# Optimization experiments

Measured on AMD Instinct MI355X. Metric: run time of the kernel, lower is better.

Reference implementation:

```python
import jax, jax.numpy as jnp
from jax import lax
import numpy as np

VOCAB = 50000
EMBED = 300
UNITS = 512          # num_nodes[0]
D1 = 1024            # num_nodes[1]
D2 = 1024            # num_nodes[2]
NUM_CLASSES = 20
B, T = 64, 512


def setup_inputs() -> dict:
    key = jax.random.key(0)
    ks = jax.random.split(key, 12)
    s = 0.02
    return {
        "tokens": jax.random.randint(ks[0], (B, T), 0, VOCAB),
        "emb": jax.random.normal(ks[1], (VOCAB, EMBED), jnp.float32) * s,
        "Wx": jax.random.normal(ks[2], (EMBED, 4 * UNITS), jnp.float32) * s,
        "Wh": jax.random.normal(ks[3], (UNITS, 4 * UNITS), jnp.float32) * s,
        "b": jnp.zeros((4 * UNITS,), jnp.float32),
        "W1": jax.random.normal(ks[4], (UNITS, D1), jnp.float32) * s,
        "b1": jnp.zeros((D1,), jnp.float32),
        "W2": jax.random.normal(ks[5], (D1, D2), jnp.float32) * s,
        "b2": jnp.zeros((D2,), jnp.float32),
        "Wo": jax.random.normal(ks[6], (D2, NUM_CLASSES), jnp.float32) * s,
        "bo": jnp.zeros((NUM_CLASSES,), jnp.float32),
    }


def reference(tokens, emb, Wx, Wh, b, W1, b1, W2, b2, Wo, bo):
    # Embedding with mask_zero=True: token 0 timesteps are masked -> LSTM skips
    # the state update (Keras semantics).
    mask = (tokens != 0)                               # [B, T]
    x = emb[tokens]                                    # [B, T, E]
    units = Wh.shape[0]
    # Precompute input contribution to the gates (parallel over time).
    xg = jnp.einsum('bte,eg->btg', x, Wx) + b          # [B, T, 4U]

    def step(carry, inp):
        h, c = carry
        g_x, m = inp                                   # [B,4U], [B]
        g = g_x + h @ Wh                               # [B, 4U]
        i, f, cc, o = jnp.split(g, 4, axis=-1)         # Keras gate order i,f,c,o
        i = jax.nn.sigmoid(i)
        f = jax.nn.sigmoid(f)
        o = jax.nn.sigmoid(o)
        # activation='relu' replaces tanh in candidate and output transform.
        c_new = f * c + i * jax.nn.relu(cc)
        h_new = o * jax.nn.relu(c_new)
        m = m[:, None]
        h = jnp.where(m, h_new, h)
        c = jnp.where(m, c_new, c)
        return (h, c), None

    h0 = jnp.zeros((tokens.shape[0], units), x.dtype)
    (h, _), _ = lax.scan(step, (h0, h0),
                         (jnp.swapaxes(xg, 0, 1), mask.T))  # scan over T

    h = jax.nn.relu(h @ W1 + b1)
    h = jax.nn.relu(h @ W2 + b2)
    return jax.nn.softmax(h @ Wo + bo)
```

## Files before the change

### kernel.cpp

```cpp
#include <hip/hip_runtime.h>
#include <hip/hip_bf16.h>

#define B_   64
#define T_   512
#define E_   300
#define U_   512
#define G4_  2048
#define D1_  1024
#define D2_  1024
#define NC_  20
#define KP_  320

typedef __bf16 bf16x8 __attribute__((ext_vector_type(8)));
typedef float  f32x4  __attribute__((ext_vector_type(4)));

__device__ __forceinline__ float sigmoidf_(float x) { return 1.0f / (1.0f + __expf(-x)); }

__device__ __forceinline__ void gl_lds16(const void* g, void* l) {
    __builtin_amdgcn_global_load_lds(
        (const __attribute__((address_space(1))) unsigned int*)g,
        (__attribute__((address_space(3))) unsigned int*)l, 16, 0, 0);
}

__global__ void init_kernel(unsigned int* __restrict__ hz, int* __restrict__ flags) {
    int idx = blockIdx.x * 256 + threadIdx.x;
    if (idx < (B_ * U_ / 2)) hz[idx] = 0u;
    if (idx < 256) flags[idx] = 0;
}

__global__ __launch_bounds__(256) void prep_wxT(const float* __restrict__ Wx,
                                                __hip_bfloat16* __restrict__ wxT) {
    __shared__ __hip_bfloat16 t[64][65];
    const int n0 = blockIdx.x * 64;
    const int k0 = blockIdx.y * 64;
    const int tid = threadIdx.x;
    for (int i = tid; i < 4096; i += 256) {
        int r = i >> 6, c = i & 63;
        int k = k0 + r;
        float v = (k < E_) ? Wx[(size_t)k * G4_ + n0 + c] : 0.f;
        t[r][c] = __float2bfloat16(v);
    }
    __syncthreads();
    for (int i = tid; i < 4096; i += 256) {
        int r = i >> 6, c = i & 63;
        wxT[(size_t)(n0 + r) * KP_ + k0 + c] = t[c][r];
    }
}

__global__ __launch_bounds__(256) void prep_xb(const int* __restrict__ tokens,
                                               const float* __restrict__ emb,
                                               __hip_bfloat16* __restrict__ xb) {
    const int row = blockIdx.x * 4 + (threadIdx.x >> 6);
    const int ln  = threadIdx.x & 63;
    const int tok = tokens[row];
    const float* src = emb + (size_t)tok * E_;
    __hip_bfloat16* dst = xb + (size_t)row * KP_;
    for (int k = ln; k < KP_; k += 64)
        dst[k] = (k < E_) ? __float2bfloat16(src[k]) : __float2bfloat16(0.f);
}

__global__ __launch_bounds__(256) void xg_gemm(const __hip_bfloat16* __restrict__ xb,
                                               const __hip_bfloat16* __restrict__ wxT,
                                               const float* __restrict__ bias,
                                               __hip_bfloat16* __restrict__ xg) {
    const int n0g = blockIdx.x * 128;
    const int bt0 = blockIdx.y * 128;
    const int tid = threadIdx.x;
    const int w   = tid >> 6;
    const int ln  = tid & 63;
    const int fn  = ln & 15;
    const int quad = ln >> 4;
    const int m0  = (w >> 1) * 64;
    const int n0w = (w & 1) * 64;

    __shared__ __align__(16) __hip_bfloat16 As[128 * 32];
    __shared__ __align__(16) __hip_bfloat16 Bs[128 * 32];

    f32x4 acc[4][4];
    #pragma unroll
    for (int im = 0; im < 4; ++im)
        #pragma unroll
        for (int in = 0; in < 4; ++in)
            acc[im][in] = (f32x4){0.f, 0.f, 0.f, 0.f};

    const __hip_bfloat16* ga = xb  + (size_t)(bt0 + w * 32 + (ln >> 2)) * KP_ + (ln & 3) * 8;
    const __hip_bfloat16* gb = wxT + (size_t)(n0g + w * 32 + (ln >> 2)) * KP_ + (ln & 3) * 8;

    for (int kt = 0; kt < KP_ / 32; ++kt) {
        gl_lds16(ga,             &As[(w * 32) * 32]);
        gl_lds16(ga + 16 * KP_,  &As[(w * 32 + 16) * 32]);
        gl_lds16(gb,             &Bs[(w * 32) * 32]);
        gl_lds16(gb + 16 * KP_,  &Bs[(w * 32 + 16) * 32]);
        ga += 32; gb += 32;
        __syncthreads();

        bf16x8 af[4], bf[4];
        #pragma unroll
        for (int im = 0; im < 4; ++im)
            af[im] = *(const bf16x8*)&As[(m0 + im * 16 + fn) * 32 + quad * 8];
        #pragma unroll
        for (int in = 0; in < 4; ++in)
            bf[in] = *(const bf16x8*)&Bs[(n0w + in * 16 + fn) * 32 + quad * 8];
        #pragma unroll
        for (int im = 0; im < 4; ++im)
            #pragma unroll
            for (int in = 0; in < 4; ++in)
                acc[im][in] = __builtin_amdgcn_mfma_f32_16x16x32_bf16(
                    af[im], bf[in], acc[im][in], 0, 0, 0);
        __syncthreads();
    }

    #pragma unroll
    for (int in = 0; in < 4; ++in) {
        const int n = n0g + n0w + in * 16 + fn;
        const float bv = bias[n];
        #pragma unroll
        for (int im = 0; im < 4; ++im) {
            #pragma unroll
            for (int r = 0; r < 4; ++r) {
                int m = bt0 + m0 + im * 16 + quad * 4 + r;
                int bb = m >> 9, tt = m & 511;
                xg[(size_t)(tt * B_ + bb) * G4_ + n] =
                    __float2bfloat16(acc[im][in][r] + bv);
            }
        }
    }
}

__global__ __launch_bounds__(256) void lstm_kernel(const __hip_bfloat16* __restrict__ xg,
                                                   const int* __restrict__ tokens,
                                                   const float* __restrict__ Wh,
                                                   __hip_bfloat16* __restrict__ hbuf,
                                                   int* __restrict__ flags) {
    const int tid  = threadIdx.x;
    const int lane = tid & 63;
    const int wave = tid >> 6;
    const int x  = blockIdx.x & 7;
    const int r_ = blockIdx.x >> 3;
    const int ub = x * 8 + (r_ & 7);
    const int g  = r_ >> 3;
    const int u0 = ub * 8;

    __shared__ __align__(16) __hip_bfloat16 whsT[32][520];
    __shared__ __align__(16) __hip_bfloat16 hs[16][520];
    __shared__ float gbuf[16][32];
    __shared__ unsigned mask_lds[16][16];

    for (int idx = tid; idx < 32 * 512; idx += 256) {
        int c = idx & 31, k = idx >> 5;
        int col = ((c >> 3) << 9) + u0 + (c & 7);
        whsT[c][k] = __float2bfloat16(Wh[(size_t)k * G4_ + col]);
    }
    {
        int m = tid >> 4, wi = tid & 15;
        const int4* tp = (const int4*)(tokens + (size_t)(g * 16 + m) * T_ + wi * 32);
        unsigned bits = 0;
        #pragma unroll
        for (int q = 0; q < 8; ++q) {
            int4 v = tp[q];
            bits |= (v.x != 0 ? 1u : 0u) << (q * 4 + 0);
            bits |= (v.y != 0 ? 1u : 0u) << (q * 4 + 1);
            bits |= (v.z != 0 ? 1u : 0u) << (q * 4 + 2);
            bits |= (v.w != 0 ? 1u : 0u) << (q * 4 + 3);
        }
        mask_lds[m][wi] = bits;
    }

    float c0 = 0.f, c1 = 0.f, h0 = 0.f, h1 = 0.f;
    int* gflags = flags + g * 64;

    const int fn   = lane & 15;
    const int quad = lane >> 4;
    const int fc   = wave * 16 + fn;
    const int fcol = ((fc >> 3) << 9) + u0 + (fc & 7);

    __syncthreads();

    for (int s = 0; s < T_; ++s) {
        float xv[4];
        if (wave < 2) {
            #pragma unroll
            for (int r = 0; r < 4; ++r)
                xv[r] = __bfloat162float(
                    xg[(size_t)(s * B_ + g * 16 + quad * 4 + r) * G4_ + fcol]);
        }

        if (s > 0) {
            if (tid < 64) {
                while (__hip_atomic_load(&gflags[tid], __ATOMIC_RELAXED,
                                         __HIP_MEMORY_SCOPE_AGENT) < s)
                    __builtin_amdgcn_s_sleep(2);
            }
            __syncthreads();
        }

        {
            const uint4* hp = (const uint4*)(hbuf + (size_t)((s & 1) * B_ + g * 16) * U_);
            uint4 t0, t1, t2, t3;
            asm volatile(
                "global_load_dwordx4 %0, %4, off sc0 sc1\n\t"
                "global_load_dwordx4 %1, %5, off sc0 sc1\n\t"
                "global_load_dwordx4 %2, %6, off sc0 sc1\n\t"
                "s_waitcnt vmcnt(0)\n\t"
                "global_load_dwordx4 %3, %7, off sc0 sc1\n\t"
                "s_waitcnt vmcnt(0)"
                : "=&v"(t0), "=&v"(t1), "=&v"(t2), "=&v"(t3)
                : "v"(hp + tid), "v"(hp + tid + 256), "v"(hp + tid + 512),
                  "v"(hp + tid + 768)
                : "memory");
            int i0 = tid;        *((uint4*)&hs[i0 >> 6][(i0 & 63) * 8]) = t0;
            int i1 = tid + 256;  *((uint4*)&hs[i1 >> 6][(i1 & 63) * 8]) = t1;
            int i2 = tid + 512;  *((uint4*)&hs[i2 >> 6][(i2 & 63) * 8]) = t2;
            int i3 = tid + 768;  *((uint4*)&hs[i3 >> 6][(i3 & 63) * 8]) = t3;
        }
        __syncthreads();

        if (wave < 2) {
            f32x4 acc;
            #pragma unroll
            for (int r = 0; r < 4; ++r) acc[r] = xv[r];
            const __hip_bfloat16* arow = &hs[fn][quad * 8];
            const __hip_bfloat16* brow = &whsT[fc][quad * 8];
            #pragma unroll
            for (int kk = 0; kk < 16; ++kk) {
                bf16x8 av = *(const bf16x8*)(arow + kk * 32);
                bf16x8 bv = *(const bf16x8*)(brow + kk * 32);
                acc = __builtin_amdgcn_mfma_f32_16x16x32_bf16(av, bv, acc, 0, 0, 0);
            }
            #pragma unroll
            for (int r = 0; r < 4; ++r)
                gbuf[quad * 4 + r][fc] = acc[r];
        }
        __syncthreads();

        if (tid < 64) {
            const int m  = tid >> 2;
            const int u2 = (tid & 3) << 1;
            float gi0 = sigmoidf_(gbuf[m][u2]),      gi1 = sigmoidf_(gbuf[m][u2 + 1]);
            float gf0 = sigmoidf_(gbuf[m][8 + u2]),  gf1 = sigmoidf_(gbuf[m][9 + u2]);
            float gc0 = gbuf[m][16 + u2],            gc1 = gbuf[m][17 + u2];
            float go0 = sigmoidf_(gbuf[m][24 + u2]), go1 = sigmoidf_(gbuf[m][25 + u2]);
            float cn0 = gf0 * c0 + gi0 * fmaxf(gc0, 0.f);
            float cn1 = gf1 * c1 + gi1 * fmaxf(gc1, 0.f);
            float hn0 = go0 * fmaxf(cn0, 0.f);
            float hn1 = go1 * fmaxf(cn1, 0.f);
            if ((mask_lds[m][s >> 5] >> (s & 31)) & 1u) {
                c0 = cn0; c1 = cn1; h0 = hn0; h1 = hn1;
            }
            __hip_bfloat162 hv;
            hv.x = __float2bfloat16(h0);
            hv.y = __float2bfloat16(h1);
            unsigned wv;
            __builtin_memcpy(&wv, &hv, 4);
            unsigned* dst = (unsigned*)hbuf +
                (((((s + 1) & 1) * B_ + g * 16 + m) * U_ + u0 + u2) >> 1);
            __hip_atomic_store(dst, wv, __ATOMIC_RELAXED, __HIP_MEMORY_SCOPE_AGENT);
        }
        __syncthreads();
        if (tid == 0)
            __hip_atomic_store(&gflags[ub], s + 1, __ATOMIC_RELAXED,
                               __HIP_MEMORY_SCOPE_AGENT);
    }
}

__global__ __launch_bounds__(256) void fc1_kernel(const __hip_bfloat16* __restrict__ h,
                                                  const float* __restrict__ W,
                                                  const float* __restrict__ bias,
                                                  float* __restrict__ y) {
    int b = blockIdx.x >> 2, ch = blockIdx.x & 3;
    __shared__ float xrow[U_];
    for (int i = threadIdx.x; i < U_; i += 256)
        xrow[i] = __bfloat162float(h[b * U_ + i]);
    __syncthreads();
    int n = ch * 256 + threadIdx.x;
    float acc = 0.f;
    #pragma unroll 4
    for (int k = 0; k < U_; ++k) acc = fmaf(xrow[k], W[(size_t)k * D1_ + n], acc);
    y[b * D1_ + n] = fmaxf(acc + bias[n], 0.f);
}

__global__ __launch_bounds__(256) void fc2_kernel(const float* __restrict__ x,
                                                  const float* __restrict__ W,
                                                  const float* __restrict__ bias,
                                                  float* __restrict__ y) {
    int b = blockIdx.x >> 2, ch = blockIdx.x & 3;
    __shared__ float xrow[D1_];
    for (int i = threadIdx.x; i < D1_; i += 256) xrow[i] = x[b * D1_ + i];
    __syncthreads();
    int n = ch * 256 + threadIdx.x;
    float acc = 0.f;
    #pragma unroll 4
    for (int k = 0; k < D1_; ++k) acc = fmaf(xrow[k], W[(size_t)k * D2_ + n], acc);
    y[b * D2_ + n] = fmaxf(acc + bias[n], 0.f);
}

__global__ __launch_bounds__(64) void out_kernel(const float* __restrict__ h2,
                                                 const float* __restrict__ Wo,
                                                 const float* __restrict__ bo,
                                                 float* __restrict__ out) {
    int b = blockIdx.x;
    __shared__ float xrow[D2_];
    __shared__ float lg[NC_];
    __shared__ float red[2];
    for (int i = threadIdx.x; i < D2_; i += 64) xrow[i] = h2[b * D2_ + i];
    __syncthreads();
    if (threadIdx.x < NC_) {
        float a = bo[threadIdx.x];
        for (int k = 0; k < D2_; ++k) a = fmaf(xrow[k], Wo[k * NC_ + threadIdx.x], a);
        lg[threadIdx.x] = a;
    }
    __syncthreads();
    if (threadIdx.x == 0) {
        float mx = lg[0];
        for (int c = 1; c < NC_; ++c) mx = fmaxf(mx, lg[c]);
        float sm = 0.f;
        for (int c = 0; c < NC_; ++c) sm += expf(lg[c] - mx);
        red[0] = mx; red[1] = 1.0f / sm;
    }
    __syncthreads();
    if (threadIdx.x < NC_)
        out[b * NC_ + threadIdx.x] = expf(lg[threadIdx.x] - red[0]) * red[1];
}

extern "C" void kernel_launch(void* const* d_in, const int* in_sizes, int n_in,
                              void* d_out, int out_size, void* d_ws, size_t ws_size,
                              hipStream_t stream) {
    const int*   tokens = (const int*)d_in[0];
    const float* emb    = (const float*)d_in[1];
    const float* Wx     = (const float*)d_in[2];
    const float* Wh     = (const float*)d_in[3];
    const float* b      = (const float*)d_in[4];
    const float* W1     = (const float*)d_in[5];
    const float* b1     = (const float*)d_in[6];
    const float* W2     = (const float*)d_in[7];
    const float* b2     = (const float*)d_in[8];
    const float* Wo     = (const float*)d_in[9];
    const float* bo     = (const float*)d_in[10];
    float* out = (float*)d_out;

    char* ws = (char*)d_ws;
    const size_t XG_BYTES   = (size_t)T_ * B_ * G4_ * 2;
    const size_t HBUF_BYTES = (size_t)2 * B_ * U_ * 2;
    __hip_bfloat16* xg   = (__hip_bfloat16*)ws;
    __hip_bfloat16* hbuf = (__hip_bfloat16*)(ws + XG_BYTES);
    int* flags           = (int*)(ws + XG_BYTES + HBUF_BYTES);
    char* p = ws + XG_BYTES + HBUF_BYTES + 1024;
    float* h1            = (float*)p;                 p += (size_t)B_ * D1_ * 4;
    float* h2            = (float*)p;                 p += (size_t)B_ * D2_ * 4;
    __hip_bfloat16* xb   = (__hip_bfloat16*)p;        p += (size_t)B_ * T_ * KP_ * 2;
    __hip_bfloat16* wxT  = (__hip_bfloat16*)p;

    init_kernel<<<64, 256, 0, stream>>>((unsigned int*)hbuf, flags);
    prep_wxT<<<dim3(32, 5), 256, 0, stream>>>(Wx, wxT);
    prep_xb<<<(B_ * T_) / 4, 256, 0, stream>>>(tokens, emb, xb);
    xg_gemm<<<dim3(16, 256), 256, 0, stream>>>(xb, wxT, b, xg);
    lstm_kernel<<<256, 256, 0, stream>>>(xg, tokens, Wh, hbuf, flags);
    fc1_kernel<<<256, 256, 0, stream>>>(hbuf, W1, b1, h1);
    fc2_kernel<<<256, 256, 0, stream>>>(h1, W2, b2, h2);
    out_kernel<<<64, 64, 0, stream>>>(h2, Wo, bo, out);
}
```

Before: 1.655 ms.

## Replace per-block flag barrier with step-tagged hidden-state words in LSTM

Each hidden-state word now carries the timestep it belongs to, written as a 64-bit atomic store. Consumer blocks spin directly on the h data until every tag matches the step. This removes the separate flag polling, the extra block barrier and the flag store on every timestep, cutting round-trip latency in the cross-block recurrence. In exchange the exchange buffer doubles in size, every poll moves more bytes, and correctness depends on the 64-bit stores being observed atomically.

```diff
diff --git a/kernel.cpp b/kernel.cpp
--- a/kernel.cpp
+++ b/kernel.cpp
@@ -22,10 +22,10 @@
         (__attribute__((address_space(3))) unsigned int*)l, 16, 0, 0);
 }
 
-__global__ void init_kernel(unsigned int* __restrict__ hz, int* __restrict__ flags) {
+__global__ void init_kernel(uint4* __restrict__ hch) {
     int idx = blockIdx.x * 256 + threadIdx.x;
-    if (idx < (B_ * U_ / 2)) hz[idx] = 0u;
-    if (idx < 256) flags[idx] = 0;
+    int g = idx >> 11, j = idx & 2047;
+    hch[(size_t)g * 4096 + j] = (uint4){0u, 0u, 0u, 0u};
 }
 
 __global__ __launch_bounds__(256) void prep_wxT(const float* __restrict__ Wx,
@@ -94,19 +94,19 @@
         ga += 32; gb += 32;
         __syncthreads();
 
-        bf16x8 af[4], bf[4];
+        bf16x8 af[4], bfr[4];
         #pragma unroll
         for (int im = 0; im < 4; ++im)
             af[im] = *(const bf16x8*)&As[(m0 + im * 16 + fn) * 32 + quad * 8];
         #pragma unroll
         for (int in = 0; in < 4; ++in)
-            bf[in] = *(const bf16x8*)&Bs[(n0w + in * 16 + fn) * 32 + quad * 8];
+            bfr[in] = *(const bf16x8*)&Bs[(n0w + in * 16 + fn) * 32 + quad * 8];
         #pragma unroll
         for (int im = 0; im < 4; ++im)
             #pragma unroll
             for (int in = 0; in < 4; ++in)
                 acc[im][in] = __builtin_amdgcn_mfma_f32_16x16x32_bf16(
-                    af[im], bf[in], acc[im][in], 0, 0, 0);
+                    af[im], bfr[in], acc[im][in], 0, 0, 0);
         __syncthreads();
     }
 
@@ -130,8 +130,8 @@
 __global__ __launch_bounds__(256) void lstm_kernel(const __hip_bfloat16* __restrict__ xg,
                                                    const int* __restrict__ tokens,
                                                    const float* __restrict__ Wh,
-                                                   __hip_bfloat16* __restrict__ hbuf,
-                                                   int* __restrict__ flags) {
+                                                   uint4* __restrict__ hch,
+                                                   __hip_bfloat16* __restrict__ hfin) {
     const int tid  = threadIdx.x;
     const int lane = tid & 63;
     const int wave = tid >> 6;
@@ -166,8 +166,15 @@
         mask_lds[m][wi] = bits;
     }
 
-    float c0 = 0.f, c1 = 0.f, h0 = 0.f, h1 = 0.f;
-    int* gflags = flags + g * 64;
+    float cst[4] = {0.f, 0.f, 0.f, 0.f};
+    float hst[4] = {0.f, 0.f, 0.f, 0.f};
+    const int um = tid >> 1;
+    const int uu = (tid & 1) * 4;
+
+    const int sm  = tid >> 4;
+    const int sjb = tid & 15;
+
+    uint4* gbase = hch + (size_t)g * 4096;
 
     const int fn   = lane & 15;
     const int quad = lane >> 4;
@@ -185,33 +192,40 @@
                     xg[(size_t)(s * B_ + g * 16 + quad * 4 + r) * G4_ + fcol]);
         }
 
-        if (s > 0) {
-            if (tid < 64) {
-                while (__hip_atomic_load(&gflags[tid], __ATOMIC_RELAXED,
-                                         __HIP_MEMORY_SCOPE_AGENT) < s)
-                    __builtin_amdgcn_s_sleep(2);
+        {
+            const uint4* cp = gbase + (s & 1) * 2048 + sm * 128 + sjb;
+            uint4 v0, v1, v2, v3, v4, v5, v6, v7;
+            const unsigned exp = (unsigned)s;
+            for (;;) {
+                asm volatile(
+                    "global_load_dwordx4 %0, %8, off sc0 sc1\n\t"
+                    "global_load_dwordx4 %1, %8, off offset:256 sc0 sc1\n\t"
+                    "global_load_dwordx4 %2, %8, off offset:512 sc0 sc1\n\t"
+                    "global_load_dwordx4 %3, %8, off offset:768 sc0 sc1\n\t"
+                    "global_load_dwordx4 %4, %8, off offset:1024 sc0 sc1\n\t"
+                    "global_load_dwordx4 %5, %8, off offset:1280 sc0 sc1\n\t"
+                    "global_load_dwordx4 %6, %8, off offset:1536 sc0 sc1\n\t"
+                    "global_load_dwordx4 %7, %8, off offset:1792 sc0 sc1\n\t"
+                    "s_waitcnt vmcnt(0)"
+                    : "=&v"(v0), "=&v"(v1), "=&v"(v2), "=&v"(v3),
+                      "=&v"(v4), "=&v"(v5), "=&v"(v6), "=&v"(v7)
+                    : "v"(cp)
+                    : "memory");
+                bool ok = (v0.y == exp) & (v0.w == exp) & (v1.y == exp) & (v1.w == exp)
+                        & (v2.y == exp) & (v2.w == exp) & (v3.y == exp) & (v3.w == exp)
+                        & (v4.y == exp) & (v4.w == exp) & (v5.y == exp) & (v5.w == exp)
+                        & (v6.y == exp) & (v6.w == exp) & (v7.y == exp) & (v7.w == exp);
+                if (ok) break;
+                __builtin_amdgcn_s_sleep(1);
             }
-            __syncthreads();
-        }
-
-        {
-            const uint4* hp = (const uint4*)(hbuf + (size_t)((s & 1) * B_ + g * 16) * U_);
-            uint4 t0, t1, t2, t3;
-            asm volatile(
-                "global_load_dwordx4 %0, %4, off sc0 sc1\n\t"
-                "global_load_dwordx4 %1, %5, off sc0 sc1\n\t"
-                "global_load_dwordx4 %2, %6, off sc0 sc1\n\t"
-                "s_waitcnt vmcnt(0)\n\t"
-                "global_load_dwordx4 %3, %7, off sc0 sc1\n\t"
-                "s_waitcnt vmcnt(0)"
-                : "=&v"(t0), "=&v"(t1), "=&v"(t2), "=&v"(t3)
-                : "v"(hp + tid), "v"(hp + tid + 256), "v"(hp + tid + 512),
-                  "v"(hp + tid + 768)
-                : "memory");
-            int i0 = tid;        *((uint4*)&hs[i0 >> 6][(i0 & 63) * 8]) = t0;
-            int i1 = tid + 256;  *((uint4*)&hs[i1 >> 6][(i1 & 63) * 8]) = t1;
-            int i2 = tid + 512;  *((uint4*)&hs[i2 >> 6][(i2 & 63) * 8]) = t2;
-            int i3 = tid + 768;  *((uint4*)&hs[i3 >> 6][(i3 & 63) * 8]) = t3;
+            *(uint2*)&hs[sm][(sjb +   0) * 4] = (uint2){v0.x, v0.z};
+            *(uint2*)&hs[sm][(sjb +  16) * 4] = (uint2){v1.x, v1.z};
+            *(uint2*)&hs[sm][(sjb +  32) * 4] = (uint2){v2.x, v2.z};
+            *(uint2*)&hs[sm][(sjb +  48) * 4] = (uint2){v3.x, v3.z};
+            *(uint2*)&hs[sm][(sjb +  64) * 4] = (uint2){v4.x, v4.z};
+            *(uint2*)&hs[sm][(sjb +  80) * 4] = (uint2){v5.x, v5.z};
+            *(uint2*)&hs[sm][(sjb +  96) * 4] = (uint2){v6.x, v6.z};
+            *(uint2*)&hs[sm][(sjb + 112) * 4] = (uint2){v7.x, v7.z};
         }
         __syncthreads();
 
@@ -233,33 +247,34 @@
         }
         __syncthreads();
 
-        if (tid < 64) {
-            const int m  = tid >> 2;
-            const int u2 = (tid & 3) << 1;
-            float gi0 = sigmoidf_(gbuf[m][u2]),      gi1 = sigmoidf_(gbuf[m][u2 + 1]);
-            float gf0 = sigmoidf_(gbuf[m][8 + u2]),  gf1 = sigmoidf_(gbuf[m][9 + u2]);
-            float gc0 = gbuf[m][16 + u2],            gc1 = gbuf[m][17 + u2];
-            float go0 = sigmoidf_(gbuf[m][24 + u2]), go1 = sigmoidf_(gbuf[m][25 + u2]);
-            float cn0 = gf0 * c0 + gi0 * fmaxf(gc0, 0.f);
-            float cn1 = gf1 * c1 + gi1 * fmaxf(gc1, 0.f);
-            float hn0 = go0 * fmaxf(cn0, 0.f);
-            float hn1 = go1 * fmaxf(cn1, 0.f);
-            if ((mask_lds[m][s >> 5] >> (s & 31)) & 1u) {
-                c0 = cn0; c1 = cn1; h0 = hn0; h1 = hn1;
+        if (tid < 32) {
+            const unsigned m = mask_lds[um][s >> 5] >> (s & 31) & 1u;
+            #pragma unroll
+            for (int q = 0; q < 4; ++q) {
+                float gi = sigmoidf_(gbuf[um][uu + q]);
+                float gf = sigmoidf_(gbuf[um][8 + uu + q]);
+                float gc = gbuf[um][16 + uu + q];
+                float go = sigmoidf_(gbuf[um][24 + uu + q]);
+                float cn = gf * cst[q] + gi * fmaxf(gc, 0.f);
+                float hn = go * fmaxf(cn, 0.f);
+                if (m) { cst[q] = cn; hst[q] = hn; }
             }
-            __hip_bfloat162 hv;
-            hv.x = __float2bfloat16(h0);
-            hv.y = __float2bfloat16(h1);
-            unsigned wv;
-            __builtin_memcpy(&wv, &hv, 4);
-            unsigned* dst = (unsigned*)hbuf +
-                (((((s + 1) & 1) * B_ + g * 16 + m) * U_ + u0 + u2) >> 1);
-            __hip_atomic_store(dst, wv, __ATOMIC_RELAXED, __HIP_MEMORY_SCOPE_AGENT);
-        }
-        __syncthreads();
-        if (tid == 0)
-            __hip_atomic_store(&gflags[ub], s + 1, __ATOMIC_RELAXED,
-                               __HIP_MEMORY_SCOPE_AGENT);
+            __hip_bfloat162 p0, p1;
+            p0.x = __float2bfloat16(hst[0]); p0.y = __float2bfloat16(hst[1]);
+            p1.x = __float2bfloat16(hst[2]); p1.y = __float2bfloat16(hst[3]);
+            unsigned d0, d1;
+            __builtin_memcpy(&d0, &p0, 4);
+            __builtin_memcpy(&d1, &p1, 4);
+            const unsigned long long tagw = (unsigned long long)(unsigned)(s + 1) << 32;
+            unsigned long long h01 = tagw | d0;
+            unsigned long long h23 = tagw | d1;
+            unsigned long long* dst = (unsigned long long*)
+                (gbase + ((s + 1) & 1) * 2048 + um * 128 + ub * 2 + (tid & 1));
+            __hip_atomic_store(dst,     h01, __ATOMIC_RELAXED, __HIP_MEMORY_SCOPE_AGENT);
+            __hip_atomic_store(dst + 1, h23, __ATOMIC_RELAXED, __HIP_MEMORY_SCOPE_AGENT);
+            if (s == T_ - 1)
+                *(uint2*)&hfin[(size_t)(g * 16 + um) * U_ + u0 + uu] = (uint2){d0, d1};
+        }
     }
 }
 
@@ -339,23 +354,24 @@
     float* out = (float*)d_out;
 
     char* ws = (char*)d_ws;
-    const size_t XG_BYTES   = (size_t)T_ * B_ * G4_ * 2;
-    const size_t HBUF_BYTES = (size_t)2 * B_ * U_ * 2;
+    const size_t XG_BYTES  = (size_t)T_ * B_ * G4_ * 2;
+    const size_t CH_BYTES  = (size_t)4 * 2 * 2048 * 16;
+    const size_t HF_BYTES  = (size_t)B_ * U_ * 2;
     __hip_bfloat16* xg   = (__hip_bfloat16*)ws;
-    __hip_bfloat16* hbuf = (__hip_bfloat16*)(ws + XG_BYTES);
-    int* flags           = (int*)(ws + XG_BYTES + HBUF_BYTES);
-    char* p = ws + XG_BYTES + HBUF_BYTES + 1024;
+    uint4* hch           = (uint4*)(ws + XG_BYTES);
+    __hip_bfloat16* hfin = (__hip_bfloat16*)(ws + XG_BYTES + CH_BYTES);
+    char* p = ws + XG_BYTES + CH_BYTES + HF_BYTES;
     float* h1            = (float*)p;                 p += (size_t)B_ * D1_ * 4;
     float* h2            = (float*)p;                 p += (size_t)B_ * D2_ * 4;
     __hip_bfloat16* xb   = (__hip_bfloat16*)p;        p += (size_t)B_ * T_ * KP_ * 2;
     __hip_bfloat16* wxT  = (__hip_bfloat16*)p;
 
-    init_kernel<<<64, 256, 0, stream>>>((unsigned int*)hbuf, flags);
+    init_kernel<<<32, 256, 0, stream>>>(hch);
     prep_wxT<<<dim3(32, 5), 256, 0, stream>>>(Wx, wxT);
     prep_xb<<<(B_ * T_) / 4, 256, 0, stream>>>(tokens, emb, xb);
     xg_gemm<<<dim3(16, 256), 256, 0, stream>>>(xb, wxT, b, xg);
-    lstm_kernel<<<256, 256, 0, stream>>>(xg, tokens, Wh, hbuf, flags);
-    fc1_kernel<<<256, 256, 0, stream>>>(hbuf, W1, b1, h1);
+    lstm_kernel<<<256, 256, 0, stream>>>(xg, tokens, Wh, hch, hfin);
+    fc1_kernel<<<256, 256, 0, stream>>>(hfin, W1, b1, h1);
     fc2_kernel<<<256, 256, 0, stream>>>(h1, W2, b2, h2);
     out_kernel<<<64, 64, 0, stream>>>(h2, Wo, bo, out);
 }
```

Measured after the change: 2.929 ms. 77.0% more time.
